# Kernel optimization log

Measured on AMD Instinct MI355X. Metric: run time of the kernel, lower is better.

Reference implementation:

```python
import jax, jax.numpy as jnp
import numpy as np

B, S, D, H = 2, 2048, 2048, 16
HD = D // H
WHERE_CONST = -10000.0

def setup_inputs() -> dict:
    key = jax.random.key(0)
    k1, k2, k3 = jax.random.split(key, 3)
    x = jax.random.normal(k1, (B, S, D), dtype=jnp.float32)
    attention_mask = jnp.zeros((B, 1, 1, S), dtype=jnp.float32)
    w_qkv = jax.random.normal(k2, (D, 3 * D), dtype=jnp.float32) * (1.0 / np.sqrt(D))
    b_qkv = jnp.zeros((3 * D,), dtype=jnp.float32)
    w_dense = jax.random.normal(k3, (D, D), dtype=jnp.float32) * (1.0 / np.sqrt(D))
    b_dense = jnp.zeros((D,), dtype=jnp.float32)
    return {"x": x, "attention_mask": attention_mask, "w_qkv": w_qkv,
            "b_qkv": b_qkv, "w_dense": w_dense, "b_dense": b_dense}

def reference(x, attention_mask, w_qkv, b_qkv, w_dense, b_dense):
    # fused QKV projection: [B,S,3D]
    qkv = jnp.einsum('bsd,de->bse', x, w_qkv) + b_qkv
    # [B,S,H,3*hd] -> [B,H,S,3*hd]
    qkv = qkv.reshape(B, S, H, 3 * HD).transpose(0, 2, 1, 3)
    q, k, v = jnp.split(qkv, 3, axis=-1)  # each [B,H,S,hd]
    # scores [B,H,S,S], scaled
    scores = jnp.einsum('bhqd,bhkd->bhqk', q, k) / np.sqrt(HD)
    causal = jnp.tril(jnp.ones((S, S), dtype=bool))[None, None]
    scores = jnp.where(causal, scores, WHERE_CONST)
    scores = scores + attention_mask
    probs = jax.nn.softmax(scores, axis=-1)
    # attention dropout is identity in eval mode
    ctx = jnp.einsum('bhqk,bhkd->bhqd', probs, v)  # [B,H,S,hd]
    ctx = ctx.transpose(0, 2, 1, 3).reshape(B, S, D)
    out = jnp.einsum('bsd,de->bse', ctx, w_dense) + b_dense
    # output dropout is identity in eval mode
    return out
```

## Files before the change

### kernel.cpp

```cpp
#include <hip/hip_runtime.h>
#include <hip/hip_bf16.h>

typedef __bf16 bf16x8 __attribute__((ext_vector_type(8)));
typedef float f32x4 __attribute__((ext_vector_type(4)));
typedef float f32x16 __attribute__((ext_vector_type(16)));
typedef unsigned short u16;

#define S_ 2048
#define D_ 2048
#define H_ 16
#define HD_ 128
#define SCALE_ 0.08838834764831845f

__device__ __forceinline__ u16 f2bf(float f) {
  unsigned u = __builtin_bit_cast(unsigned, f);
  u += 0x7fffu + ((u >> 16) & 1u);
  return (u16)(u >> 16);
}

__device__ __forceinline__ void gload16(void* lds, const void* g) {
  __builtin_amdgcn_global_load_lds((const __attribute__((address_space(1))) void*)g,
                                   (__attribute__((address_space(3))) void*)lds, 16, 0, 0);
}

__device__ __forceinline__ f32x4 mfma16(bf16x8 a, bf16x8 b, f32x4 c) {
  return __builtin_amdgcn_mfma_f32_16x16x32_bf16(a, b, c, 0, 0, 0);
}
__device__ __forceinline__ f32x16 mfma32(bf16x8 a, bf16x8 b, f32x16 c) {
  return __builtin_amdgcn_mfma_f32_32x32x16_bf16(a, b, c, 0, 0, 0);
}

__device__ __forceinline__ unsigned cvt_pk_bf16(float lo, float hi) {
  unsigned r;
  asm("v_cvt_pk_bf16_f32 %0, %1, %2" : "=v"(r) : "v"(lo), "v"(hi));
  return r;
}

__global__ void k_cast_bf16(const float* __restrict__ in, u16* __restrict__ out, int n4) {
  int i = blockIdx.x * blockDim.x + threadIdx.x;
  if (i < n4) {
    float4 v = ((const float4*)in)[i];
    ushort4 o;
    o.x = f2bf(v.x); o.y = f2bf(v.y); o.z = f2bf(v.z); o.w = f2bf(v.w);
    ((ushort4*)out)[i] = o;
  }
}

__global__ void k_transpose_cast(const float* __restrict__ in, u16* __restrict__ out,
                                 int rows, int cols) {
  __shared__ u16 tile[32][33];
  int c0 = blockIdx.x * 32, r0 = blockIdx.y * 32;
  int tx = threadIdx.x, ty = threadIdx.y;
#pragma unroll
  for (int i = 0; i < 4; i++) {
    int r = r0 + ty + i * 8;
    tile[ty + i * 8][tx] = f2bf(in[(long)r * cols + c0 + tx]);
  }
  __syncthreads();
#pragma unroll
  for (int i = 0; i < 4; i++) {
    int c = c0 + ty + i * 8;
    out[(long)c * rows + r0 + tx] = tile[tx][ty + i * 8];
  }
}

__device__ __forceinline__ void qkv_store(u16* __restrict__ qb, u16* __restrict__ kpk,
                                          u16* __restrict__ vpk, int row, int col, float val) {
  u16 o = f2bf(val);
  int h = col / 384;
  int m3 = col - h * 384;
  int b = row >> 11, s = row & 2047;
  int bh = b * 16 + h, t = s >> 5;
  if (m3 < 128) {
    qb[(long)row * 2048 + h * 128 + m3] = o;
  } else if (m3 < 256) {
    int dd = m3 - 128;
    long idx = ((((long)bh * 64 + t) * 8 + (dd >> 4)) * 64 + (((dd >> 3) & 1) << 5) + (s & 31)) * 8 + (dd & 7);
    kpk[idx] = o;
  } else {
    int dd = m3 - 256;
    long idx = ((((long)bh * 64 + t) * 8 + (((s >> 4) & 1) << 2) + (dd >> 5)) * 64 + (((s >> 3) & 1) << 5) + (dd & 31)) * 8 + (s & 7);
    vpk[idx] = o;
  }
}

template <int MODE>
__global__ __launch_bounds__(512) void k_gemm2(const u16* __restrict__ A,
                                               const u16* __restrict__ Bt,
                                               const float* __restrict__ bias,
                                               void* __restrict__ Cv,
                                               int M, int N, int K, int NTM,
                                               u16* __restrict__ qb,
                                               u16* __restrict__ kpk,
                                               u16* __restrict__ vpk) {
  __shared__ __align__(16) u16 lA[2][256 * 64];
  __shared__ __align__(16) u16 lB[2][128 * 64];
  const int tid = threadIdx.x, w = tid >> 6, l = tid & 63;
  const int wr = w >> 1, wc = w & 1, lr = l & 15, lg = l >> 4;
  const int nwg = NTM * (N >> 7);
  const int per = nwg >> 3;
  const int wgid = ((int)blockIdx.x & 7) * per + ((int)blockIdx.x >> 3);
  const int tm = (wgid % NTM) << 8;
  const int tn = (wgid / NTM) << 7;
  const int NT = K >> 6;

  f32x4 acc[4][4];
#pragma unroll
  for (int m = 0; m < 4; m++)
#pragma unroll
    for (int n = 0; n < 4; n++) acc[m][n] = {0.f, 0.f, 0.f, 0.f};

  auto stageA = [&](int buf, int kt) {
#pragma unroll
    for (int i = 0; i < 4; i++) {
      int base = i * 512 + w * 64;
      int fl = base + l, r = fl >> 3, cg = (fl & 7) ^ (r & 7);
      gload16(&lA[buf][base * 8], &A[(long)(tm + r) * K + kt * 64 + cg * 8]);
    }
  };
  auto stageB = [&](int buf, int kt) {
#pragma unroll
    for (int i = 0; i < 2; i++) {
      int base = i * 512 + w * 64;
      int fl = base + l, r = fl >> 3, cg = (fl & 7) ^ (r & 7);
      gload16(&lB[buf][base * 8], &Bt[(long)(tn + r) * K + kt * 64 + cg * 8]);
    }
  };

  stageA(0, 0);
  stageB(0, 0);
  if (NT > 1) stageA(1, 1);
  asm volatile("s_waitcnt vmcnt(4)" ::: "memory");
  __builtin_amdgcn_s_barrier();

  for (int kt = 0; kt < NT; ++kt) {
    const int b = kt & 1;
    bf16x8 af[4][2], bfr[2][2];
#pragma unroll
    for (int m = 0; m < 4; m++)
#pragma unroll
      for (int k = 0; k < 2; k++) {
        int r = wr * 64 + m * 16 + lr;
        af[m][k] = *(const bf16x8*)&lA[b][r * 64 + ((((k << 2) + lg) ^ (r & 7)) << 3)];
      }
#pragma unroll
    for (int n = 0; n < 2; n++)
#pragma unroll
      for (int k = 0; k < 2; k++) {
        int r = wc * 64 + n * 16 + lr;
        bfr[n][k] = *(const bf16x8*)&lB[b][r * 64 + ((((k << 2) + lg) ^ (r & 7)) << 3)];
      }
    if (kt + 1 < NT) stageB(b ^ 1, kt + 1);
    __builtin_amdgcn_s_barrier();
    asm volatile("s_waitcnt lgkmcnt(0)" ::: "memory");
    __builtin_amdgcn_sched_barrier(0);
    __builtin_amdgcn_s_setprio(1);
#pragma unroll
    for (int m = 0; m < 4; m++)
#pragma unroll
      for (int n = 0; n < 2; n++)
#pragma unroll
        for (int k = 0; k < 2; k++)
          acc[m][n] = mfma16(af[m][k], bfr[n][k], acc[m][n]);
    __builtin_amdgcn_s_setprio(0);
    __builtin_amdgcn_s_barrier();

#pragma unroll
    for (int n = 0; n < 2; n++)
#pragma unroll
      for (int k = 0; k < 2; k++) {
        int r = wc * 64 + (n + 2) * 16 + lr;
        bfr[n][k] = *(const bf16x8*)&lB[b][r * 64 + ((((k << 2) + lg) ^ (r & 7)) << 3)];
      }
    if (kt + 2 < NT) stageA(b, kt + 2);
    __builtin_amdgcn_s_barrier();
    if (kt + 2 < NT)
      asm volatile("s_waitcnt vmcnt(4) lgkmcnt(0)" ::: "memory");
    else
      asm volatile("s_waitcnt vmcnt(0) lgkmcnt(0)" ::: "memory");
    __builtin_amdgcn_sched_barrier(0);
    __builtin_amdgcn_s_setprio(1);
#pragma unroll
    for (int m = 0; m < 4; m++)
#pragma unroll
      for (int n = 0; n < 2; n++)
#pragma unroll
        for (int k = 0; k < 2; k++)
          acc[m][n + 2] = mfma16(af[m][k], bfr[n][k], acc[m][n + 2]);
    __builtin_amdgcn_s_setprio(0);
    __builtin_amdgcn_s_barrier();
  }

#pragma unroll
  for (int n = 0; n < 4; n++) {
    int col = tn + wc * 64 + n * 16 + lr;
    float bv = bias[col];
#pragma unroll
    for (int m = 0; m < 4; m++) {
      int row0 = tm + wr * 64 + m * 16 + lg * 4;
#pragma unroll
      for (int j = 0; j < 4; j++) {
        float v = acc[m][n][j] + bv;
        if constexpr (MODE == 2)
          qkv_store(qb, kpk, vpk, row0 + j, col, v);
        else
          ((float*)Cv)[(long)(row0 + j) * N + col] = v;
      }
    }
  }
}

__global__ __launch_bounds__(256, 2) void k_attn(const u16* __restrict__ qb,
                                                 const u16* __restrict__ kpk,
                                                 const u16* __restrict__ vpk,
                                                 const float* __restrict__ amask,
                                                 u16* __restrict__ ctx) {
  const int bh = blockIdx.x, b = bh >> 4, h = bh & 15;
  const int pr = blockIdx.y;
  const int tid = threadIdx.x, w = tid >> 6, l = tid & 63;
  const int lr5 = l & 31, hi = l >> 5;
  const int qrow0 = (w < 2) ? (pr * 64 + w * 32) : ((31 - pr) * 64 + (w - 2) * 32);
  const int nt = (qrow0 >> 5) + 1;

  bf16x8 qf[8];
  {
    const u16* qp = qb + (long)(b * S_ + qrow0 + lr5) * 2048 + h * HD_ + hi * 8;
#pragma unroll
    for (int ks = 0; ks < 8; ks++) qf[ks] = *(const bf16x8*)(qp + ks * 16);
  }

  f32x16 aO[4];
#pragma unroll
  for (int db = 0; db < 4; db++)
#pragma unroll
    for (int r = 0; r < 16; r++) aO[db][r] = 0.f;
  float mrun = -3.0e38f, lrun = 0.f;

  const u16* kbase = kpk + (long)bh * 64 * 8 * 512 + l * 8;
  const u16* vbase = vpk + (long)bh * 64 * 8 * 512 + l * 8;
  const float* ab0 = amask + b * S_;

  bf16x8 kA[8], kB[8];
#pragma unroll
  for (int f = 0; f < 8; f++) kA[f] = *(const bf16x8*)(kbase + f * 512);

  auto body = [&](bf16x8 (&cur)[8], bf16x8 (&nxt)[8], int t) {
    const int t32 = t << 5;
    bf16x8 vf[8];
    {
      const u16* vp = vbase + (long)t * 4096;
#pragma unroll
      for (int f = 0; f < 8; f++) vf[f] = *(const bf16x8*)(vp + f * 512);
    }
    f32x4 am[4];
#pragma unroll
    for (int rg = 0; rg < 4; rg++) am[rg] = *(const f32x4*)(ab0 + t32 + rg * 8 + hi * 4);

    f32x16 aS;
#pragma unroll
    for (int r = 0; r < 16; r++) aS[r] = 0.f;
    __builtin_amdgcn_s_setprio(1);
#pragma unroll
    for (int ks = 0; ks < 8; ks++) aS = mfma32(cur[ks], qf[ks], aS);
    __builtin_amdgcn_s_setprio(0);

    if (t + 1 < nt) {
      const u16* kp = kbase + (long)(t + 1) * 4096;
#pragma unroll
      for (int f = 0; f < 8; f++) nxt[f] = *(const bf16x8*)(kp + f * 512);
    }

    float v[16];
    const bool needmask = (t == (qrow0 >> 5));
#pragma unroll
    for (int rg = 0; rg < 4; rg++)
#pragma unroll
      for (int j = 0; j < 4; j++) {
        v[rg * 4 + j] = fmaf(aS[rg * 4 + j], SCALE_, am[rg][j]);
        if (needmask && (rg * 8 + hi * 4 + j > lr5)) v[rg * 4 + j] = -1e30f;
      }
    float mx = v[0];
#pragma unroll
    for (int i = 1; i < 16; i++) mx = fmaxf(mx, v[i]);
    mx = fmaxf(mx, __shfl_xor(mx, 32));

    if (!__all(mx <= mrun + 8.0f)) {
      float mnew = fmaxf(mrun, mx);
      float corr = __expf(mrun - mnew);
      lrun *= corr;
      mrun = mnew;
#pragma unroll
      for (int reg = 0; reg < 16; reg++) {
        float cb = __shfl(corr, (reg & 3) + 8 * (reg >> 2) + 4 * hi);
#pragma unroll
        for (int db = 0; db < 4; db++) aO[db][reg] *= cb;
      }
    }

    float ls = 0.f;
#pragma unroll
    for (int i = 0; i < 16; i++) { v[i] = __expf(v[i] - mrun); ls += v[i]; }
    ls += __shfl_xor(ls, 32);
    lrun += ls;

    unsigned pk[8];
#pragma unroll
    for (int q = 0; q < 8; q++) pk[q] = cvt_pk_bf16(v[2 * q], v[2 * q + 1]);
    bf16x8 pa[2];
#pragma unroll
    for (int kst = 0; kst < 2; kst++) {
      unsigned a0 = pk[4 * kst], a1 = pk[4 * kst + 1], a2 = pk[4 * kst + 2], a3 = pk[4 * kst + 3];
      unsigned s0 = hi ? a0 : a2;
      unsigned s1 = hi ? a1 : a3;
      unsigned r0 = __shfl_xor(s0, 32);
      unsigned r1 = __shfl_xor(s1, 32);
      union { unsigned u[4]; bf16x8 vv; } U;
      U.u[0] = hi ? r0 : a0;
      U.u[1] = hi ? r1 : a1;
      U.u[2] = hi ? a2 : r0;
      U.u[3] = hi ? a3 : r1;
      pa[kst] = U.vv;
    }

    __builtin_amdgcn_s_setprio(1);
#pragma unroll
    for (int kst = 0; kst < 2; kst++)
#pragma unroll
      for (int db = 0; db < 4; db++)
        aO[db] = mfma32(pa[kst], vf[kst * 4 + db], aO[db]);
    __builtin_amdgcn_s_setprio(0);
  };

  for (int t = 0; t < nt; t += 2) {
    body(kA, kB, t);
    if (t + 1 < nt) body(kB, kA, t + 1);
  }

  float inv = 1.0f / lrun;
#pragma unroll
  for (int reg = 0; reg < 16; reg++) {
    int r = (reg & 3) + 8 * (reg >> 2) + 4 * hi;
    float ib = __shfl(inv, r);
    int srow = qrow0 + r;
#pragma unroll
    for (int db = 0; db < 4; db++)
      ctx[(long)(b * S_ + srow) * D_ + h * HD_ + db * 32 + lr5] = f2bf(aO[db][reg] * ib);
  }
}

extern "C" void kernel_launch(void* const* d_in, const int* in_sizes, int n_in,
                              void* d_out, int out_size, void* d_ws, size_t ws_size,
                              hipStream_t stream) {
  const float* x  = (const float*)d_in[0];
  const float* am = (const float*)d_in[1];
  const float* wq = (const float*)d_in[2];
  const float* bq = (const float*)d_in[3];
  const float* wd = (const float*)d_in[4];
  const float* bd = (const float*)d_in[5];
  float* out = (float*)d_out;
  char* ws = (char*)d_ws;

  const size_t MB = 1048576;
  u16* xb   = (u16*)(ws);
  u16* wqT  = (u16*)(ws + 16 * MB);
  u16* qb   = (u16*)(ws + 40 * MB);
  u16* kpk  = (u16*)(ws + 56 * MB);
  u16* vpk  = (u16*)(ws + 72 * MB);
  u16* ctxb = (u16*)(ws);
  u16* wdT  = (u16*)(ws + 16 * MB);

  k_cast_bf16<<<8192, 256, 0, stream>>>(x, xb, 2097152);
  k_transpose_cast<<<dim3(192, 64), dim3(32, 8), 0, stream>>>(wq, wqT, 2048, 6144);
  k_gemm2<2><<<768, 512, 0, stream>>>(xb, wqT, bq, nullptr, 4096, 6144, 2048, 16, qb, kpk, vpk);
  k_transpose_cast<<<dim3(64, 64), dim3(32, 8), 0, stream>>>(wd, wdT, 2048, 2048);
  k_attn<<<dim3(32, 16), 256, 0, stream>>>(qb, kpk, vpk, am, ctxb);
  k_gemm2<0><<<256, 512, 0, stream>>>(ctxb, wdT, bd, (void*)out, 4096, 2048, 2048, 16,
                                      nullptr, nullptr, nullptr);
}
```

Measured before the change: 264.5 us.

## Use 256x256 tile GEMM with interleaved half-tile staging for QKV projection

Adds a new GEMM kernel with 256x256 output tiles per workgroup (8 waves as 2x4, each wave 128x64) and uses it for the QKV projection, halving the workgroup count from 768 to 384. Global-to-LDS loads for the next K step are split into half-tile stages placed between four MFMA phases, with barriers and vmcnt waits throughout. The larger tile raises arithmetic intensity and operand reuse per LDS load. In exchange it doubles accumulator registers and uses more LDS. The output GEMM is kept on the old kernel, now specialised without the template mode.

New measurement: 271.0 us. 2.4% more time.

```diff
diff --git a/kernel.cpp b/kernel.cpp
--- a/kernel.cpp
+++ b/kernel.cpp
@@ -85,7 +85,7 @@
 }
 
 template <int MODE>
-__global__ __launch_bounds__(512) void k_gemm2(const u16* __restrict__ A,
+__global__ __launch_bounds__(512) void k_gemm8(const u16* __restrict__ A,
                                                const u16* __restrict__ Bt,
                                                const float* __restrict__ bias,
                                                void* __restrict__ Cv,
@@ -93,6 +93,164 @@
                                                u16* __restrict__ qb,
                                                u16* __restrict__ kpk,
                                                u16* __restrict__ vpk) {
+  __shared__ __align__(16) u16 lA[2][2][128 * 64];
+  __shared__ __align__(16) u16 lB[2][2][128 * 64];
+  const int tid = threadIdx.x, w = tid >> 6, l = tid & 63;
+  const int wm = w >> 2, wn = w & 3, lr = l & 15, lg = l >> 4;
+  const int nwg = NTM * (N >> 8);
+  const int per = nwg >> 3;
+  const int wgid = ((int)blockIdx.x & 7) * per + ((int)blockIdx.x >> 3);
+  const int tm = (wgid % NTM) << 8;
+  const int tn = (wgid / NTM) << 8;
+  const int NT = K >> 6;
+
+  f32x4 acc[8][4];
+#pragma unroll
+  for (int m = 0; m < 8; m++)
+#pragma unroll
+    for (int n = 0; n < 4; n++) acc[m][n] = {0.f, 0.f, 0.f, 0.f};
+
+  auto stageAh = [&](int kt, int hf) {
+    int s = kt & 1;
+#pragma unroll
+    for (int i = 0; i < 2; i++) {
+      int f = i * 512 + tid, r = f >> 3, cg = (f & 7) ^ (r & 7);
+      gload16(&lA[s][hf][(i * 512 + w * 64) * 8],
+              &A[(long)(tm + hf * 128 + r) * K + kt * 64 + cg * 8]);
+    }
+  };
+  auto stageBh = [&](int kt, int hf) {
+    int s = kt & 1;
+#pragma unroll
+    for (int i = 0; i < 2; i++) {
+      int f = i * 512 + tid, r = f >> 3, cg = (f & 7) ^ (r & 7);
+      gload16(&lB[s][hf][(i * 512 + w * 64) * 8],
+              &Bt[(long)(tn + hf * 128 + r) * K + kt * 64 + cg * 8]);
+    }
+  };
+
+  stageAh(0, 0); stageAh(0, 1);
+  stageBh(0, 0); stageBh(0, 1);
+  if (NT > 1) { stageBh(1, 0); stageBh(1, 1); }
+  asm volatile("s_waitcnt vmcnt(4)" ::: "memory");
+  __builtin_amdgcn_s_barrier();
+
+  auto half_iter = [&](int s, int ktA, bool gA, int ktB, bool gB) {
+    bf16x8 aL[4][2], aH[4][2], b01[2][2], b23[2][2];
+#pragma unroll
+    for (int m = 0; m < 4; m++)
+#pragma unroll
+      for (int k = 0; k < 2; k++) {
+        int rr = m * 16 + lr;
+        aL[m][k] = *(const bf16x8*)&lA[s][wm][rr * 64 + ((((k << 2) + lg) ^ (rr & 7)) << 3)];
+      }
+#pragma unroll
+    for (int n = 0; n < 2; n++)
+#pragma unroll
+      for (int k = 0; k < 2; k++) {
+        int rb = (wn & 1) * 64 + n * 16 + lr;
+        b01[n][k] = *(const bf16x8*)&lB[s][wn >> 1][rb * 64 + ((((k << 2) + lg) ^ (rb & 7)) << 3)];
+      }
+    if (gA) stageAh(ktA, 0);
+    __builtin_amdgcn_s_barrier();
+    asm volatile("s_waitcnt lgkmcnt(0)" ::: "memory");
+    __builtin_amdgcn_sched_barrier(0);
+    __builtin_amdgcn_s_setprio(1);
+#pragma unroll
+    for (int m = 0; m < 4; m++)
+#pragma unroll
+      for (int n = 0; n < 2; n++)
+#pragma unroll
+        for (int k = 0; k < 2; k++) acc[m][n] = mfma16(aL[m][k], b01[n][k], acc[m][n]);
+    __builtin_amdgcn_s_setprio(0);
+    __builtin_amdgcn_s_barrier();
+#pragma unroll
+    for (int n = 0; n < 2; n++)
+#pragma unroll
+      for (int k = 0; k < 2; k++) {
+        int rb = (wn & 1) * 64 + (n + 2) * 16 + lr;
+        b23[n][k] = *(const bf16x8*)&lB[s][wn >> 1][rb * 64 + ((((k << 2) + lg) ^ (rb & 7)) << 3)];
+      }
+    if (gA) stageAh(ktA, 1);
+    __builtin_amdgcn_s_barrier();
+    asm volatile("s_waitcnt lgkmcnt(0)" ::: "memory");
+    __builtin_amdgcn_sched_barrier(0);
+    __builtin_amdgcn_s_setprio(1);
+#pragma unroll
+    for (int m = 0; m < 4; m++)
+#pragma unroll
+      for (int n = 0; n < 2; n++)
+#pragma unroll
+        for (int k = 0; k < 2; k++) acc[m][n + 2] = mfma16(aL[m][k], b23[n][k], acc[m][n + 2]);
+    __builtin_amdgcn_s_setprio(0);
+    __builtin_amdgcn_s_barrier();
+#pragma unroll
+    for (int m = 0; m < 4; m++)
+#pragma unroll
+      for (int k = 0; k < 2; k++) {
+        int rr = 64 + m * 16 + lr;
+        aH[m][k] = *(const bf16x8*)&lA[s][wm][rr * 64 + ((((k << 2) + lg) ^ (rr & 7)) << 3)];
+      }
+    if (gB) stageBh(ktB, 0);
+    __builtin_amdgcn_s_barrier();
+    asm volatile("s_waitcnt lgkmcnt(0)" ::: "memory");
+    __builtin_amdgcn_sched_barrier(0);
+    __builtin_amdgcn_s_setprio(1);
+#pragma unroll
+    for (int m = 0; m < 4; m++)
+#pragma unroll
+      for (int n = 0; n < 2; n++)
+#pragma unroll
+        for (int k = 0; k < 2; k++) acc[m + 4][n] = mfma16(aH[m][k], b01[n][k], acc[m + 4][n]);
+    __builtin_amdgcn_s_setprio(0);
+    __builtin_amdgcn_s_barrier();
+    if (gB) stageBh(ktB, 1);
+    __builtin_amdgcn_s_barrier();
+    if (gB) asm volatile("s_waitcnt vmcnt(4)" ::: "memory");
+    else    asm volatile("s_waitcnt vmcnt(0)" ::: "memory");
+    __builtin_amdgcn_sched_barrier(0);
+    __builtin_amdgcn_s_setprio(1);
+#pragma unroll
+    for (int m = 0; m < 4; m++)
+#pragma unroll
+      for (int n = 0; n < 2; n++)
+#pragma unroll
+        for (int k = 0; k < 2; k++) acc[m + 4][n + 2] = mfma16(aH[m][k], b23[n][k], acc[m + 4][n + 2]);
+    __builtin_amdgcn_s_setprio(0);
+    __builtin_amdgcn_s_barrier();
+  };
+
+  for (int j = 0; j < (NT >> 1); ++j) {
+    const int t = 2 * j;
+    const bool g2 = (t + 2 < NT), g3 = (t + 3 < NT);
+    half_iter(0, t + 1, true, t + 2, g2);
+    half_iter(1, t + 2, g2,   t + 3, g3);
+  }
+
+#pragma unroll
+  for (int n = 0; n < 4; n++) {
+    int col = tn + wn * 64 + n * 16 + lr;
+    float bv = bias[col];
+#pragma unroll
+    for (int m = 0; m < 8; m++) {
+      int row0 = tm + wm * 128 + m * 16 + lg * 4;
+#pragma unroll
+      for (int j = 0; j < 4; j++) {
+        float v = acc[m][n][j] + bv;
+        if constexpr (MODE == 2)
+          qkv_store(qb, kpk, vpk, row0 + j, col, v);
+        else
+          ((float*)Cv)[(long)(row0 + j) * N + col] = v;
+      }
+    }
+  }
+}
+
+__global__ __launch_bounds__(512) void k_gemm2(const u16* __restrict__ A,
+                                               const u16* __restrict__ Bt,
+                                               const float* __restrict__ bias,
+                                               float* __restrict__ Cv,
+                                               int M, int N, int K, int NTM) {
   __shared__ __align__(16) u16 lA[2][256 * 64];
   __shared__ __align__(16) u16 lB[2][128 * 64];
   const int tid = threadIdx.x, w = tid >> 6, l = tid & 63;
@@ -199,13 +357,8 @@
     for (int m = 0; m < 4; m++) {
       int row0 = tm + wr * 64 + m * 16 + lg * 4;
 #pragma unroll
-      for (int j = 0; j < 4; j++) {
-        float v = acc[m][n][j] + bv;
-        if constexpr (MODE == 2)
-          qkv_store(qb, kpk, vpk, row0 + j, col, v);
-        else
-          ((float*)Cv)[(long)(row0 + j) * N + col] = v;
-      }
+      for (int j = 0; j < 4; j++)
+        Cv[(long)(row0 + j) * N + col] = acc[m][n][j] + bv;
     }
   }
 }
@@ -371,9 +524,8 @@
 
   k_cast_bf16<<<8192, 256, 0, stream>>>(x, xb, 2097152);
   k_transpose_cast<<<dim3(192, 64), dim3(32, 8), 0, stream>>>(wq, wqT, 2048, 6144);
-  k_gemm2<2><<<768, 512, 0, stream>>>(xb, wqT, bq, nullptr, 4096, 6144, 2048, 16, qb, kpk, vpk);
+  k_gemm8<2><<<384, 512, 0, stream>>>(xb, wqT, bq, nullptr, 4096, 6144, 2048, 16, qb, kpk, vpk);
   k_transpose_cast<<<dim3(64, 64), dim3(32, 8), 0, stream>>>(wd, wdT, 2048, 2048);
   k_attn<<<dim3(32, 16), 256, 0, stream>>>(qb, kpk, vpk, am, ctxb);
-  k_gemm2<0><<<256, 512, 0, stream>>>(ctxb, wdT, bd, (void*)out, 4096, 2048, 2048, 16,
-                                      nullptr, nullptr, nullptr);
-}
+  k_gemm2<<<256, 512, 0, stream>>>(ctxb, wdT, bd, out, 4096, 2048, 2048, 16);
+}
```
